# Performance work log

Hardware: AMD Instinct MI355X
Metric: run time of the kernel (lower is better)

Reference implementation:

```python
import jax, jax.numpy as jnp
import numpy as np

NEG_INF = -jnp.inf

def setup_inputs() -> dict:
    key = jax.random.key(0)
    k1, k2, k3, k4, k5 = jax.random.split(key, 5)
    b, n, d = 8, 1024, 2048
    s = 1.0 / np.sqrt(d)  # keep activations well-scaled (kaiming-ish)
    return {
        "y":  jax.random.normal(k1, (b, n, d), dtype=jnp.float32),
        "Wk": jax.random.normal(k2, (d, d), dtype=jnp.float32) * s,
        "Wq": jax.random.normal(k3, (d, d), dtype=jnp.float32) * s,
        "Wv": jax.random.normal(k4, (d, d), dtype=jnp.float32) * s,
        "Wo": jax.random.normal(k5, (d, d), dtype=jnp.float32) * s,
    }

def reference(y, Wk, Wq, Wv, Wo):
    # nn.Linear(bias=False): x @ W.T
    K = jnp.einsum('bnd,ed->bne', y, Wk)
    Q = 0.1 * jnp.einsum('bnd,ed->bne', y, Wq)
    V = jnp.einsum('bnd,ed->bne', y, Wv)
    # logits[b,i,j] = Q_i . K_j
    logits = jnp.einsum('bid,bjd->bij', Q, K)
    n = y.shape[1]
    diag = jnp.eye(n, dtype=bool)  # self-exclusion mask on the diagonal
    logits = jnp.where(diag[None, :, :], NEG_INF, logits)
    # NOTE: softmax over dim=1 (rows of the score matrix), non-standard axis
    attention_weights = jax.nn.softmax(logits, axis=1)
    # dropout(p=0.5) treated as identity (eval/deterministic reference)
    # torch: (V^T @ W)^T  ==  out[b,i,:] = sum_j W[b,j,i] * V[b,j,:]
    out = jnp.einsum('bji,bjd->bid', attention_weights, V)
    out = jnp.einsum('bid,ed->bie', out, Wo)
    return (out, attention_weights)
```

## Files before the change

kernel.cpp:

```cpp
#include <hip/hip_runtime.h>

typedef unsigned short u16;
typedef __attribute__((ext_vector_type(8))) __bf16 bf16x8;
typedef __attribute__((ext_vector_type(4))) float f32x4;
typedef __attribute__((ext_vector_type(4))) unsigned short u16x4;
typedef __attribute__((ext_vector_type(8))) unsigned short u16x8;

#define GLOBAL_AS __attribute__((address_space(1)))
#define LDS_AS __attribute__((address_space(3)))

__device__ __forceinline__ void gload_lds16(const void* g, void* l) {
    __builtin_amdgcn_global_load_lds((const GLOBAL_AS void*)g, (LDS_AS void*)l, 16, 0, 0);
}

__device__ __forceinline__ u16 f2bf(float f) {
    union { float f; unsigned u; } x; x.f = f;
    unsigned r = x.u + 0x7FFFu + ((x.u >> 16) & 1u);
    return (u16)(r >> 16);
}
__device__ __forceinline__ float bf2f(u16 h) {
    union { unsigned u; float f; } x; x.u = ((unsigned)h) << 16;
    return x.f;
}
struct BfPair { u16 h, l; };
__device__ __forceinline__ BfPair split2(float v) {
    BfPair p;
    p.h = f2bf(v);
    p.l = f2bf(v - bf2f(p.h));
    return p;
}

#define TM 128
#define TN 128
#define BK 64

__global__ __launch_bounds__(256) void conv_bf(
    const float* __restrict__ src, u16* __restrict__ dst, int n8)
{
    const int stride = gridDim.x * 256;
    for (int i = blockIdx.x * 256 + threadIdx.x; i < n8; i += stride) {
        const float* g = src + (size_t)i * 8;
        f32x4 v0 = *(const f32x4*)g;
        f32x4 v1 = *(const f32x4*)(g + 4);
        u16x8 w;
        #pragma unroll
        for (int e = 0; e < 4; ++e) { w[e] = f2bf(v0[e]); w[e + 4] = f2bf(v1[e]); }
        *(u16x8*)(dst + (size_t)i * 8) = w;
    }
}

__global__ __launch_bounds__(256) void transpose_conv(
    const float* __restrict__ S, u16* __restrict__ D)
{
    __shared__ float tile[64][65];
    const int x0 = blockIdx.x * 64;
    const int y0 = blockIdx.y * 64;
    const int t = threadIdx.x;
    const int rt = t >> 4;
    const int c4 = (t & 15) * 4;

    #pragma unroll
    for (int p = 0; p < 4; ++p) {
        const int r = p * 16 + rt;
        f32x4 v = *(const f32x4*)(S + (size_t)(y0 + r) * 2048 + x0 + c4);
        #pragma unroll
        for (int e = 0; e < 4; ++e) tile[r][c4 + e] = v[e];
    }
    __syncthreads();
    #pragma unroll
    for (int p = 0; p < 4; ++p) {
        const int a = p * 16 + rt;
        u16x4 w;
        #pragma unroll
        for (int e = 0; e < 4; ++e) w[e] = f2bf(tile[c4 + e][a]);
        *(u16x4*)(D + (size_t)(x0 + a) * 2048 + y0 + c4) = w;
    }
}

template <bool OSPLIT>
__global__ __launch_bounds__(256) void gemm_bf(
    const u16* __restrict__ A, const u16* __restrict__ B,
    u16* __restrict__ Ch, u16* __restrict__ Cl,
    int M, int N, int K, size_t sAb, size_t sBb, size_t sCb, float alpha)
{
    __shared__ u16 As[TM * BK];
    __shared__ u16 Bs[TN * BK];

    const int z = blockIdx.z;
    const u16* Ab = (const u16*)((const char*)A + (size_t)z * sAb);
    const u16* Bb = (const u16*)((const char*)B + (size_t)z * sBb);

    const int n0 = blockIdx.x * TN;
    const int m0 = blockIdx.y * TM;
    const int tid = threadIdx.x;
    const int lane = tid & 63;
    const int wave = tid >> 6;
    const int wm = (wave >> 1) * 64;
    const int wn = (wave & 1) * 64;
    const int quad = lane >> 4;
    const int lrow = lane & 15;

    f32x4 acc[4][4] = {};

    for (int k0 = 0; k0 < K; k0 += BK) {
        #pragma unroll
        for (int r = 0; r < 4; ++r) {
            const int wbase = r * 4096 + wave * 1024;
            const int o = wbase + lane * 16;
            const int row = o >> 7;
            const int ce = (o & 127) >> 1;
            const size_t ao = (size_t)(m0 + row) * K + k0 + ce;
            const size_t bo = (size_t)(n0 + row) * K + k0 + ce;
            gload_lds16(Ab + ao, (char*)As + wbase);
            gload_lds16(Bb + bo, (char*)Bs + wbase);
        }
        __syncthreads();

        #pragma unroll
        for (int kk = 0; kk < BK; kk += 32) {
            bf16x8 af[4], bfr[4];
            #pragma unroll
            for (int t = 0; t < 4; ++t) {
                af[t]  = *(const bf16x8*)&As[(wm + t * 16 + lrow) * BK + kk + quad * 8];
                bfr[t] = *(const bf16x8*)&Bs[(wn + t * 16 + lrow) * BK + kk + quad * 8];
            }
            #pragma unroll
            for (int ti = 0; ti < 4; ++ti)
                #pragma unroll
                for (int tj = 0; tj < 4; ++tj)
                    acc[ti][tj] = __builtin_amdgcn_mfma_f32_16x16x32_bf16(
                        af[ti], bfr[tj], acc[ti][tj], 0, 0, 0);
        }
        __syncthreads();
    }

    u16* Chb = (u16*)((char*)Ch + (size_t)z * sCb);
    u16* Clb = OSPLIT ? (u16*)((char*)Cl + (size_t)z * sCb) : nullptr;
    #pragma unroll
    for (int ti = 0; ti < 4; ++ti)
        #pragma unroll
        for (int tj = 0; tj < 4; ++tj) {
            const int nn = n0 + wn + tj * 16 + lrow;
            #pragma unroll
            for (int r2 = 0; r2 < 4; ++r2) {
                const int mm = m0 + wm + ti * 16 + quad * 4 + r2;
                if (OSPLIT) {
                    BfPair p = split2(acc[ti][tj][r2] * alpha);
                    Chb[(size_t)mm * N + nn] = p.h;
                    Clb[(size_t)mm * N + nn] = p.l;
                } else {
                    Chb[(size_t)mm * N + nn] = f2bf(acc[ti][tj][r2] * alpha);
                }
            }
        }
}

__global__ __launch_bounds__(256) void gemm_ll(
    const u16* __restrict__ Ah, const u16* __restrict__ Al,
    const u16* __restrict__ Bh, const u16* __restrict__ Bl,
    float* __restrict__ C,
    int M, int N, int K, size_t sAb, size_t sBb, size_t sCb)
{
    __shared__ u16 Ash[TM * BK];
    __shared__ u16 Asl[TM * BK];
    __shared__ u16 Bsh[TN * BK];
    __shared__ u16 Bsl[TN * BK];

    const int z = blockIdx.z;
    const u16* Ahb = (const u16*)((const char*)Ah + (size_t)z * sAb);
    const u16* Alb = (const u16*)((const char*)Al + (size_t)z * sAb);
    const u16* Bhb = (const u16*)((const char*)Bh + (size_t)z * sBb);
    const u16* Blb = (const u16*)((const char*)Bl + (size_t)z * sBb);

    const int n0 = blockIdx.x * TN;
    const int m0 = blockIdx.y * TM;
    const int tid = threadIdx.x;
    const int lane = tid & 63;
    const int wave = tid >> 6;
    const int wm = (wave >> 1) * 64;
    const int wn = (wave & 1) * 64;
    const int quad = lane >> 4;
    const int lrow = lane & 15;

    f32x4 acc[4][4] = {};

    for (int k0 = 0; k0 < K; k0 += BK) {
        #pragma unroll
        for (int r = 0; r < 4; ++r) {
            const int wbase = r * 4096 + wave * 1024;
            const int o = wbase + lane * 16;
            const int row = o >> 7;
            const int ce = (o & 127) >> 1;
            const size_t ao = (size_t)(m0 + row) * K + k0 + ce;
            const size_t bo = (size_t)(n0 + row) * K + k0 + ce;
            gload_lds16(Ahb + ao, (char*)Ash + wbase);
            gload_lds16(Alb + ao, (char*)Asl + wbase);
            gload_lds16(Bhb + bo, (char*)Bsh + wbase);
            gload_lds16(Blb + bo, (char*)Bsl + wbase);
        }
        __syncthreads();

        #pragma unroll
        for (int kk = 0; kk < BK; kk += 32) {
            bf16x8 ah[4], al[4], bh[4], bl[4];
            #pragma unroll
            for (int t = 0; t < 4; ++t) {
                const int ra = (wm + t * 16 + lrow) * BK + kk + quad * 8;
                const int rb = (wn + t * 16 + lrow) * BK + kk + quad * 8;
                ah[t] = *(const bf16x8*)&Ash[ra];
                al[t] = *(const bf16x8*)&Asl[ra];
                bh[t] = *(const bf16x8*)&Bsh[rb];
                bl[t] = *(const bf16x8*)&Bsl[rb];
            }
            #pragma unroll
            for (int ti = 0; ti < 4; ++ti)
                #pragma unroll
                for (int tj = 0; tj < 4; ++tj) {
                    acc[ti][tj] = __builtin_amdgcn_mfma_f32_16x16x32_bf16(
                        al[ti], bh[tj], acc[ti][tj], 0, 0, 0);
                    acc[ti][tj] = __builtin_amdgcn_mfma_f32_16x16x32_bf16(
                        ah[ti], bl[tj], acc[ti][tj], 0, 0, 0);
                    acc[ti][tj] = __builtin_amdgcn_mfma_f32_16x16x32_bf16(
                        ah[ti], bh[tj], acc[ti][tj], 0, 0, 0);
                }
        }
        __syncthreads();
    }

    float* Cb = (float*)((char*)C + (size_t)z * sCb);
    #pragma unroll
    for (int ti = 0; ti < 4; ++ti)
        #pragma unroll
        for (int tj = 0; tj < 4; ++tj) {
            const int nn = n0 + wn + tj * 16 + lrow;
            #pragma unroll
            for (int r2 = 0; r2 < 4; ++r2) {
                const int mm = m0 + wm + ti * 16 + quad * 4 + r2;
                Cb[(size_t)mm * N + nn] = acc[ti][tj][r2];
            }
        }
}

__global__ __launch_bounds__(256) void gemm_fin(
    const u16* __restrict__ Ah, const u16* __restrict__ Al,
    const u16* __restrict__ B, float* __restrict__ C,
    int M, int N, int K, size_t sAb, size_t sBb, size_t sCb)
{
    __shared__ u16 Ash[TM * BK];
    __shared__ u16 Asl[TM * BK];
    __shared__ u16 Bs[TN * BK];

    const int z = blockIdx.z;
    const u16* Ahb = (const u16*)((const char*)Ah + (size_t)z * sAb);
    const u16* Alb = (const u16*)((const char*)Al + (size_t)z * sAb);
    const u16* Bb  = (const u16*)((const char*)B + (size_t)z * sBb);

    const int n0 = blockIdx.x * TN;
    const int m0 = blockIdx.y * TM;
    const int tid = threadIdx.x;
    const int lane = tid & 63;
    const int wave = tid >> 6;
    const int wm = (wave >> 1) * 64;
    const int wn = (wave & 1) * 64;
    const int quad = lane >> 4;
    const int lrow = lane & 15;

    f32x4 acc[4][4] = {};

    for (int k0 = 0; k0 < K; k0 += BK) {
        #pragma unroll
        for (int r = 0; r < 4; ++r) {
            const int wbase = r * 4096 + wave * 1024;
            const int o = wbase + lane * 16;
            const int row = o >> 7;
            const int ce = (o & 127) >> 1;
            const size_t ao = (size_t)(m0 + row) * K + k0 + ce;
            const size_t bo = (size_t)(n0 + row) * K + k0 + ce;
            gload_lds16(Ahb + ao, (char*)Ash + wbase);
            gload_lds16(Alb + ao, (char*)Asl + wbase);
            gload_lds16(Bb + bo, (char*)Bs + wbase);
        }
        __syncthreads();

        #pragma unroll
        for (int kk = 0; kk < BK; kk += 32) {
            bf16x8 ah[4], al[4], bfr[4];
            #pragma unroll
            for (int t = 0; t < 4; ++t) {
                const int ra = (wm + t * 16 + lrow) * BK + kk + quad * 8;
                ah[t] = *(const bf16x8*)&Ash[ra];
                al[t] = *(const bf16x8*)&Asl[ra];
                bfr[t] = *(const bf16x8*)&Bs[(wn + t * 16 + lrow) * BK + kk + quad * 8];
            }
            #pragma unroll
            for (int ti = 0; ti < 4; ++ti)
                #pragma unroll
                for (int tj = 0; tj < 4; ++tj) {
                    acc[ti][tj] = __builtin_amdgcn_mfma_f32_16x16x32_bf16(
                        al[ti], bfr[tj], acc[ti][tj], 0, 0, 0);
                    acc[ti][tj] = __builtin_amdgcn_mfma_f32_16x16x32_bf16(
                        ah[ti], bfr[tj], acc[ti][tj], 0, 0, 0);
                }
        }
        __syncthreads();
    }

    float* Cb = (float*)((char*)C + (size_t)z * sCb);
    #pragma unroll
    for (int ti = 0; ti < 4; ++ti)
        #pragma unroll
        for (int tj = 0; tj < 4; ++tj) {
            const int nn = n0 + wn + tj * 16 + lrow;
            #pragma unroll
            for (int r2 = 0; r2 < 4; ++r2) {
                const int mm = m0 + wm + ti * 16 + quad * 4 + r2;
                Cb[(size_t)mm * N + nn] = acc[ti][tj][r2];
            }
        }
}

__global__ __launch_bounds__(256) void softmax_split(
    const float* __restrict__ Lh, u16* __restrict__ Th, u16* __restrict__ Tl)
{
    const int lane = threadIdx.x & 63;
    const int wave = threadIdx.x >> 6;
    const size_t row = (size_t)blockIdx.x * 4 + wave;
    const int i = (int)(row & 1023);
    const float* src = Lh + row * 1024;
    const float NEG = -__builtin_inff();

    float v[16];
    float mx = NEG;
    #pragma unroll
    for (int cc = 0; cc < 4; ++cc) {
        f32x4 x = *(const f32x4*)(src + cc * 256 + lane * 4);
        #pragma unroll
        for (int e = 0; e < 4; ++e) {
            const int j = cc * 256 + lane * 4 + e;
            const float val = (j == i) ? NEG : x[e];
            v[cc * 4 + e] = val;
            mx = fmaxf(mx, val);
        }
    }
    #pragma unroll
    for (int off = 32; off > 0; off >>= 1) mx = fmaxf(mx, __shfl_xor(mx, off, 64));
    float s = 0.f;
    #pragma unroll
    for (int k = 0; k < 16; ++k) { v[k] = __expf(v[k] - mx); s += v[k]; }
    #pragma unroll
    for (int off = 32; off > 0; off >>= 1) s += __shfl_xor(s, off, 64);
    const float inv = 1.0f / s;

    #pragma unroll
    for (int cc = 0; cc < 4; ++cc) {
        u16x4 wh, wl;
        #pragma unroll
        for (int e = 0; e < 4; ++e) {
            BfPair p = split2(v[cc * 4 + e] * inv);
            wh[e] = p.h;
            wl[e] = p.l;
        }
        *(u16x4*)(Th + row * 1024 + cc * 256 + lane * 4) = wh;
        *(u16x4*)(Tl + row * 1024 + cc * 256 + lane * 4) = wl;
    }
}

__global__ __launch_bounds__(256) void transpose_attn_f32(
    const u16* __restrict__ Th, const u16* __restrict__ Tl, float* __restrict__ A)
{
    __shared__ float tile[64][65];
    const int bz = blockIdx.z;
    const int x0 = blockIdx.x * 64;
    const int y0 = blockIdx.y * 64;
    const size_t base = (size_t)bz * 1024 * 1024;
    float* dst = A + base;
    const int t = threadIdx.x;
    const int rt = t >> 4;
    const int c4 = (t & 15) * 4;

    #pragma unroll
    for (int p = 0; p < 4; ++p) {
        const int r = p * 16 + rt;
        const size_t off = base + (size_t)(y0 + r) * 1024 + x0 + c4;
        u16x4 vh = *(const u16x4*)(Th + off);
        u16x4 vl = *(const u16x4*)(Tl + off);
        #pragma unroll
        for (int e = 0; e < 4; ++e) tile[r][c4 + e] = bf2f(vh[e]) + bf2f(vl[e]);
    }
    __syncthreads();
    #pragma unroll
    for (int p = 0; p < 4; ++p) {
        const int a = p * 16 + rt;
        f32x4 w;
        #pragma unroll
        for (int e = 0; e < 4; ++e) w[e] = tile[c4 + e][a];
        *(f32x4*)(dst + (size_t)(x0 + a) * 1024 + y0 + c4) = w;
    }
}

extern "C" void kernel_launch(void* const* d_in, const int* in_sizes, int n_in,
                              void* d_out, int out_size, void* d_ws, size_t ws_size,
                              hipStream_t stream) {
    const float* y  = (const float*)d_in[0];
    const float* Wk = (const float*)d_in[1];
    const float* Wq = (const float*)d_in[2];
    const float* Wv = (const float*)d_in[3];
    const float* Wo = (const float*)d_in[4];

    const int b = 8, n = 1024, d = 2048;
    const int MB = b * n;
    const size_t MiB = 1024 * 1024;

    char* ws = (char*)d_ws;
    u16* yB   = (u16*)(ws);
    u16* UtB  = (u16*)(ws + 32 * MiB);
    u16* Kh   = (u16*)(ws + 40 * MiB);
    u16* Kl   = (u16*)(ws + 72 * MiB);
    u16* WkB  = (u16*)(ws + 104 * MiB);
    u16* WqB  = (u16*)(ws + 112 * MiB);
    u16* WoB  = (u16*)(ws + 120 * MiB);
    u16* Th   = (u16*)(ws + 40 * MiB);
    u16* Tl   = (u16*)(ws + 56 * MiB);
    u16* VOtB = (u16*)(ws + 72 * MiB);

    float* outF = (float*)d_out;
    float* attF = outF + (size_t)MB * d;
    u16*   WvTB = (u16*)d_out;
    u16*   Qh = (u16*)d_out;
    u16*   Ql = (u16*)((char*)d_out + 32 * MiB);
    float* Lh = (float*)((char*)d_out + 64 * MiB);

    dim3 blk(256);
    conv_bf<<<dim3(2048), blk, 0, stream>>>(y,  yB,  (MB * d) / 8);
    conv_bf<<<dim3(2048), blk, 0, stream>>>(Wk, WkB, (d * d) / 8);
    conv_bf<<<dim3(2048), blk, 0, stream>>>(Wq, WqB, (d * d) / 8);
    conv_bf<<<dim3(2048), blk, 0, stream>>>(Wo, WoB, (d * d) / 8);
    transpose_conv<<<dim3(32, 32), blk, 0, stream>>>(Wv, WvTB);
    gemm_bf<false><<<dim3(d / TN, d / TM, 1), blk, 0, stream>>>(
        WoB, WvTB, UtB, nullptr, d, d, d, 0, 0, 0, 1.0f);
    gemm_bf<true><<<dim3(d / TN, MB / TM, 1), blk, 0, stream>>>(
        yB, WkB, Kh, Kl, MB, d, d, 0, 0, 0, 1.0f);
    gemm_bf<true><<<dim3(d / TN, MB / TM, 1), blk, 0, stream>>>(
        yB, WqB, Qh, Ql, MB, d, d, 0, 0, 0, 0.1f);
    gemm_ll<<<dim3(n / TN, n / TM, b), blk, 0, stream>>>(
        Kh, Kl, Qh, Ql, Lh, n, n, d,
        (size_t)n * d * 2, (size_t)n * d * 2, (size_t)n * n * 4);
    softmax_split<<<dim3(MB / 4), blk, 0, stream>>>(Lh, Th, Tl);
    transpose_attn_f32<<<dim3(16, 16, b), blk, 0, stream>>>(Th, Tl, attF);
    gemm_bf<false><<<dim3(n / TN, d / TM, b), blk, 0, stream>>>(
        UtB, yB, VOtB, nullptr, d, n, d, 0, (size_t)n * d * 2, (size_t)d * n * 2, 1.0f);
    gemm_fin<<<dim3(d / TN, n / TM, b), blk, 0, stream>>>(
        Th, Tl, VOtB, outF, n, d, n,
        (size_t)n * n * 2, (size_t)d * n * 2, (size_t)n * d * 4);
}
```

Baseline: 727.3 us.

## Fold Wq and Wk into one bilinear weight to drop a projection GEMM

Logits are computed as y·(0.1·Wq^T Wk)·y^T. The pre-combined d×d matrix G is built once, then one big GEMM forms Z = y·G (stored as a split hi/lo bf16 pair), which replaces the two separate K and Q projection GEMMs over the 8192×2048 activations. The logits GEMM now does two MFMAs per tile (bf16 y against hi/lo Z) instead of three. The small G and Wo·Wv^T precomputes are fused into one launch, and the weight transposes into another. The trade-off is extra rounding error, because y enters both sides of the logits GEMM with only a single bf16 term.

```diff
diff --git a/kernel.cpp b/kernel.cpp
--- a/kernel.cpp
+++ b/kernel.cpp
@@ -49,10 +49,14 @@
     }
 }
 
-__global__ __launch_bounds__(256) void transpose_conv(
-    const float* __restrict__ S, u16* __restrict__ D)
+__global__ __launch_bounds__(256) void transpose3(
+    const float* __restrict__ s0, const float* __restrict__ s1, const float* __restrict__ s2,
+    u16* __restrict__ d0, u16* __restrict__ d1, u16* __restrict__ d2)
 {
     __shared__ float tile[64][65];
+    const int z = blockIdx.z;
+    const float* S = (z == 0) ? s0 : (z == 1) ? s1 : s2;
+    u16* D = (z == 0) ? d0 : (z == 1) ? d1 : d2;
     const int x0 = blockIdx.x * 64;
     const int y0 = blockIdx.y * 64;
     const int t = threadIdx.x;
@@ -77,18 +81,18 @@
     }
 }
 
-template <bool OSPLIT>
-__global__ __launch_bounds__(256) void gemm_bf(
-    const u16* __restrict__ A, const u16* __restrict__ B,
-    u16* __restrict__ Ch, u16* __restrict__ Cl,
-    int M, int N, int K, size_t sAb, size_t sBb, size_t sCb, float alpha)
+__global__ __launch_bounds__(256) void gemm_pre2(
+    const u16* __restrict__ A0, const u16* __restrict__ B0,
+    u16* __restrict__ GH, u16* __restrict__ GL, float alpha0,
+    const u16* __restrict__ A1, const u16* __restrict__ B1, u16* __restrict__ U1,
+    int M, int N, int K)
 {
     __shared__ u16 As[TM * BK];
     __shared__ u16 Bs[TN * BK];
 
     const int z = blockIdx.z;
-    const u16* Ab = (const u16*)((const char*)A + (size_t)z * sAb);
-    const u16* Bb = (const u16*)((const char*)B + (size_t)z * sBb);
+    const u16* Ab = z ? A1 : A0;
+    const u16* Bb = z ? B1 : B0;
 
     const int n0 = blockIdx.x * TN;
     const int m0 = blockIdx.y * TM;
@@ -109,10 +113,82 @@
             const int o = wbase + lane * 16;
             const int row = o >> 7;
             const int ce = (o & 127) >> 1;
-            const size_t ao = (size_t)(m0 + row) * K + k0 + ce;
-            const size_t bo = (size_t)(n0 + row) * K + k0 + ce;
-            gload_lds16(Ab + ao, (char*)As + wbase);
-            gload_lds16(Bb + bo, (char*)Bs + wbase);
+            gload_lds16(Ab + (size_t)(m0 + row) * K + k0 + ce, (char*)As + wbase);
+            gload_lds16(Bb + (size_t)(n0 + row) * K + k0 + ce, (char*)Bs + wbase);
+        }
+        __syncthreads();
+
+        #pragma unroll
+        for (int kk = 0; kk < BK; kk += 32) {
+            bf16x8 af[4], bfr[4];
+            #pragma unroll
+            for (int t = 0; t < 4; ++t) {
+                af[t]  = *(const bf16x8*)&As[(wm + t * 16 + lrow) * BK + kk + quad * 8];
+                bfr[t] = *(const bf16x8*)&Bs[(wn + t * 16 + lrow) * BK + kk + quad * 8];
+            }
+            #pragma unroll
+            for (int ti = 0; ti < 4; ++ti)
+                #pragma unroll
+                for (int tj = 0; tj < 4; ++tj)
+                    acc[ti][tj] = __builtin_amdgcn_mfma_f32_16x16x32_bf16(
+                        af[ti], bfr[tj], acc[ti][tj], 0, 0, 0);
+        }
+        __syncthreads();
+    }
+
+    #pragma unroll
+    for (int ti = 0; ti < 4; ++ti)
+        #pragma unroll
+        for (int tj = 0; tj < 4; ++tj) {
+            const int nn = n0 + wn + tj * 16 + lrow;
+            #pragma unroll
+            for (int r2 = 0; r2 < 4; ++r2) {
+                const int mm = m0 + wm + ti * 16 + quad * 4 + r2;
+                if (z == 0) {
+                    BfPair p = split2(acc[ti][tj][r2] * alpha0);
+                    GH[(size_t)mm * N + nn] = p.h;
+                    GL[(size_t)mm * N + nn] = p.l;
+                } else {
+                    U1[(size_t)mm * N + nn] = f2bf(acc[ti][tj][r2]);
+                }
+            }
+        }
+}
+
+template <bool OSPLIT>
+__global__ __launch_bounds__(256) void gemm_bf(
+    const u16* __restrict__ A, const u16* __restrict__ B,
+    u16* __restrict__ Ch, u16* __restrict__ Cl,
+    int M, int N, int K, size_t sAb, size_t sBb, size_t sCb, float alpha)
+{
+    __shared__ u16 As[TM * BK];
+    __shared__ u16 Bs[TN * BK];
+
+    const int z = blockIdx.z;
+    const u16* Ab = (const u16*)((const char*)A + (size_t)z * sAb);
+    const u16* Bb = (const u16*)((const char*)B + (size_t)z * sBb);
+
+    const int n0 = blockIdx.x * TN;
+    const int m0 = blockIdx.y * TM;
+    const int tid = threadIdx.x;
+    const int lane = tid & 63;
+    const int wave = tid >> 6;
+    const int wm = (wave >> 1) * 64;
+    const int wn = (wave & 1) * 64;
+    const int quad = lane >> 4;
+    const int lrow = lane & 15;
+
+    f32x4 acc[4][4] = {};
+
+    for (int k0 = 0; k0 < K; k0 += BK) {
+        #pragma unroll
+        for (int r = 0; r < 4; ++r) {
+            const int wbase = r * 4096 + wave * 1024;
+            const int o = wbase + lane * 16;
+            const int row = o >> 7;
+            const int ce = (o & 127) >> 1;
+            gload_lds16(Ab + (size_t)(m0 + row) * K + k0 + ce, (char*)As + wbase);
+            gload_lds16(Bb + (size_t)(n0 + row) * K + k0 + ce, (char*)Bs + wbase);
         }
         __syncthreads();
 
@@ -155,20 +231,19 @@
         }
 }
 
-__global__ __launch_bounds__(256) void gemm_ll(
-    const u16* __restrict__ Ah, const u16* __restrict__ Al,
+template <bool OSPLIT>
+__global__ __launch_bounds__(256) void gemm_bs(
+    const u16* __restrict__ A,
     const u16* __restrict__ Bh, const u16* __restrict__ Bl,
-    float* __restrict__ C,
+    void* __restrict__ C, void* __restrict__ C2,
     int M, int N, int K, size_t sAb, size_t sBb, size_t sCb)
 {
-    __shared__ u16 Ash[TM * BK];
-    __shared__ u16 Asl[TM * BK];
+    __shared__ u16 As[TM * BK];
     __shared__ u16 Bsh[TN * BK];
     __shared__ u16 Bsl[TN * BK];
 
     const int z = blockIdx.z;
-    const u16* Ahb = (const u16*)((const char*)Ah + (size_t)z * sAb);
-    const u16* Alb = (const u16*)((const char*)Al + (size_t)z * sAb);
+    const u16* Ab  = (const u16*)((const char*)A + (size_t)z * sAb);
     const u16* Bhb = (const u16*)((const char*)Bh + (size_t)z * sBb);
     const u16* Blb = (const u16*)((const char*)Bl + (size_t)z * sBb);
 
@@ -193,8 +268,7 @@
             const int ce = (o & 127) >> 1;
             const size_t ao = (size_t)(m0 + row) * K + k0 + ce;
             const size_t bo = (size_t)(n0 + row) * K + k0 + ce;
-            gload_lds16(Ahb + ao, (char*)Ash + wbase);
-            gload_lds16(Alb + ao, (char*)Asl + wbase);
+            gload_lds16(Ab + ao, (char*)As + wbase);
             gload_lds16(Bhb + bo, (char*)Bsh + wbase);
             gload_lds16(Blb + bo, (char*)Bsl + wbase);
         }
@@ -202,13 +276,12 @@
 
         #pragma unroll
         for (int kk = 0; kk < BK; kk += 32) {
-            bf16x8 ah[4], al[4], bh[4], bl[4];
+            bf16x8 af[4], bh[4], bl[4];
             #pragma unroll
             for (int t = 0; t < 4; ++t) {
                 const int ra = (wm + t * 16 + lrow) * BK + kk + quad * 8;
                 const int rb = (wn + t * 16 + lrow) * BK + kk + quad * 8;
-                ah[t] = *(const bf16x8*)&Ash[ra];
-                al[t] = *(const bf16x8*)&Asl[ra];
+                af[t] = *(const bf16x8*)&As[ra];
                 bh[t] = *(const bf16x8*)&Bsh[rb];
                 bl[t] = *(const bf16x8*)&Bsl[rb];
             }
@@ -217,28 +290,44 @@
                 #pragma unroll
                 for (int tj = 0; tj < 4; ++tj) {
                     acc[ti][tj] = __builtin_amdgcn_mfma_f32_16x16x32_bf16(
-                        al[ti], bh[tj], acc[ti][tj], 0, 0, 0);
+                        af[ti], bl[tj], acc[ti][tj], 0, 0, 0);
                     acc[ti][tj] = __builtin_amdgcn_mfma_f32_16x16x32_bf16(
-                        ah[ti], bl[tj], acc[ti][tj], 0, 0, 0);
-                    acc[ti][tj] = __builtin_amdgcn_mfma_f32_16x16x32_bf16(
-                        ah[ti], bh[tj], acc[ti][tj], 0, 0, 0);
+                        af[ti], bh[tj], acc[ti][tj], 0, 0, 0);
                 }
         }
         __syncthreads();
     }
 
-    float* Cb = (float*)((char*)C + (size_t)z * sCb);
-    #pragma unroll
-    for (int ti = 0; ti < 4; ++ti)
-        #pragma unroll
-        for (int tj = 0; tj < 4; ++tj) {
-            const int nn = n0 + wn + tj * 16 + lrow;
-            #pragma unroll
-            for (int r2 = 0; r2 < 4; ++r2) {
-                const int mm = m0 + wm + ti * 16 + quad * 4 + r2;
-                Cb[(size_t)mm * N + nn] = acc[ti][tj][r2];
-            }
-        }
+    if (OSPLIT) {
+        u16* Chb = (u16*)((char*)C + (size_t)z * sCb);
+        u16* Clb = (u16*)((char*)C2 + (size_t)z * sCb);
+        #pragma unroll
+        for (int ti = 0; ti < 4; ++ti)
+            #pragma unroll
+            for (int tj = 0; tj < 4; ++tj) {
+                const int nn = n0 + wn + tj * 16 + lrow;
+                #pragma unroll
+                for (int r2 = 0; r2 < 4; ++r2) {
+                    const int mm = m0 + wm + ti * 16 + quad * 4 + r2;
+                    BfPair p = split2(acc[ti][tj][r2]);
+                    Chb[(size_t)mm * N + nn] = p.h;
+                    Clb[(size_t)mm * N + nn] = p.l;
+                }
+            }
+    } else {
+        float* Cb = (float*)((char*)C + (size_t)z * sCb);
+        #pragma unroll
+        for (int ti = 0; ti < 4; ++ti)
+            #pragma unroll
+            for (int tj = 0; tj < 4; ++tj) {
+                const int nn = n0 + wn + tj * 16 + lrow;
+                #pragma unroll
+                for (int r2 = 0; r2 < 4; ++r2) {
+                    const int mm = m0 + wm + ti * 16 + quad * 4 + r2;
+                    Cb[(size_t)mm * N + nn] = acc[ti][tj][r2];
+                }
+            }
+    }
 }
 
 __global__ __launch_bounds__(256) void gemm_fin(
@@ -412,44 +501,40 @@
     const size_t MiB = 1024 * 1024;
 
     char* ws = (char*)d_ws;
-    u16* yB   = (u16*)(ws);
-    u16* UtB  = (u16*)(ws + 32 * MiB);
-    u16* Kh   = (u16*)(ws + 40 * MiB);
-    u16* Kl   = (u16*)(ws + 72 * MiB);
-    u16* WkB  = (u16*)(ws + 104 * MiB);
-    u16* WqB  = (u16*)(ws + 112 * MiB);
-    u16* WoB  = (u16*)(ws + 120 * MiB);
-    u16* Th   = (u16*)(ws + 40 * MiB);
-    u16* Tl   = (u16*)(ws + 56 * MiB);
-    u16* VOtB = (u16*)(ws + 72 * MiB);
+    u16* yB  = (u16*)(ws);
+    u16* WkT = (u16*)(ws + 32 * MiB);
+    u16* WqT = (u16*)(ws + 40 * MiB);
+    u16* WvT = (u16*)(ws + 48 * MiB);
+    u16* WoB = (u16*)(ws + 56 * MiB);
+    u16* GtH = (u16*)(ws + 64 * MiB);
+    u16* GtL = (u16*)(ws + 72 * MiB);
+    u16* UtB = (u16*)(ws + 80 * MiB);
+    u16* ZcH = (u16*)(ws + 32 * MiB);
+    u16* ZcL = (u16*)(ws + 88 * MiB);
+    u16* Th  = (u16*)(ws + 32 * MiB);
+    u16* Tl  = (u16*)(ws + 48 * MiB);
+    u16* VOt = (u16*)(ws + 88 * MiB);
 
     float* outF = (float*)d_out;
     float* attF = outF + (size_t)MB * d;
-    u16*   WvTB = (u16*)d_out;
-    u16*   Qh = (u16*)d_out;
-    u16*   Ql = (u16*)((char*)d_out + 32 * MiB);
-    float* Lh = (float*)((char*)d_out + 64 * MiB);
+    float* Lh   = (float*)d_out;
 
     dim3 blk(256);
     conv_bf<<<dim3(2048), blk, 0, stream>>>(y,  yB,  (MB * d) / 8);
-    conv_bf<<<dim3(2048), blk, 0, stream>>>(Wk, WkB, (d * d) / 8);
-    conv_bf<<<dim3(2048), blk, 0, stream>>>(Wq, WqB, (d * d) / 8);
-    conv_bf<<<dim3(2048), blk, 0, stream>>>(Wo, WoB, (d * d) / 8);
-    transpose_conv<<<dim3(32, 32), blk, 0, stream>>>(Wv, WvTB);
-    gemm_bf<false><<<dim3(d / TN, d / TM, 1), blk, 0, stream>>>(
-        WoB, WvTB, UtB, nullptr, d, d, d, 0, 0, 0, 1.0f);
-    gemm_bf<true><<<dim3(d / TN, MB / TM, 1), blk, 0, stream>>>(
-        yB, WkB, Kh, Kl, MB, d, d, 0, 0, 0, 1.0f);
-    gemm_bf<true><<<dim3(d / TN, MB / TM, 1), blk, 0, stream>>>(
-        yB, WqB, Qh, Ql, MB, d, d, 0, 0, 0, 0.1f);
-    gemm_ll<<<dim3(n / TN, n / TM, b), blk, 0, stream>>>(
-        Kh, Kl, Qh, Ql, Lh, n, n, d,
+    conv_bf<<<dim3(512),  blk, 0, stream>>>(Wo, WoB, (d * d) / 8);
+    transpose3<<<dim3(32, 32, 3), blk, 0, stream>>>(Wk, Wq, Wv, WkT, WqT, WvT);
+    gemm_pre2<<<dim3(d / TN, d / TM, 2), blk, 0, stream>>>(
+        WkT, WqT, GtH, GtL, 0.1f, WoB, WvT, UtB, d, d, d);
+    gemm_bs<true><<<dim3(d / TN, MB / TM, 1), blk, 0, stream>>>(
+        yB, GtH, GtL, ZcH, ZcL, MB, d, d, 0, 0, 0);
+    gemm_bs<false><<<dim3(n / TN, n / TM, b), blk, 0, stream>>>(
+        yB, ZcH, ZcL, Lh, nullptr, n, n, d,
         (size_t)n * d * 2, (size_t)n * d * 2, (size_t)n * n * 4);
     softmax_split<<<dim3(MB / 4), blk, 0, stream>>>(Lh, Th, Tl);
     transpose_attn_f32<<<dim3(16, 16, b), blk, 0, stream>>>(Th, Tl, attF);
     gemm_bf<false><<<dim3(n / TN, d / TM, b), blk, 0, stream>>>(
-        UtB, yB, VOtB, nullptr, d, n, d, 0, (size_t)n * d * 2, (size_t)d * n * 2, 1.0f);
+        UtB, yB, VOt, nullptr, d, n, d, 0, (size_t)n * d * 2, (size_t)d * n * 2, 1.0f);
     gemm_fin<<<dim3(d / TN, n / TM, b), blk, 0, stream>>>(
-        Th, Tl, VOtB, outF, n, d, n,
+        Th, Tl, VOt, outF, n, d, n,
         (size_t)n * n * 2, (size_t)d * n * 2, (size_t)n * d * 4);
 }
```

Result: faster. 656.8 us (-9.7%).
